# Kernel optimization log

Measured on AMD Instinct MI355X. Metric: run time of the kernel, lower is better.

## Reference

```python
import jax, jax.numpy as jnp
import numpy as np

LENGTHSCALES = np.array([0.1, 0.2, 0.5, 1.0, 2.0, 5.0, 10.0, 20.0], dtype=np.float32)
VALUE_DIM = 64
OUTPUT_DIM = 512
NUM_HEADS = len(LENGTHSCALES)


def setup_inputs() -> dict:
    key = jax.random.key(0)
    k1, k2, k3, k4, k5 = jax.random.split(key, 5)
    B, Lq, Lk, D = 4, 2048, 2048, 3
    query_positions = jax.random.normal(k1, (B, Lq, D), dtype=jnp.float32)
    key_positions = jax.random.normal(k2, (B, Lk, D), dtype=jnp.float32)
    values = jax.random.normal(k3, (B, Lk, NUM_HEADS, VALUE_DIM), dtype=jnp.float32)
    masked_elements = jax.random.randint(k4, (B, Lk), 0, 2) > 0
    # nn.Linear(value_dim*num_heads, output_dim, bias=False): weight [out, in]
    fan_in = VALUE_DIM * NUM_HEADS
    w_out = jax.random.uniform(k5, (OUTPUT_DIM, fan_in), dtype=jnp.float32,
                               minval=-1.0, maxval=1.0) / jnp.sqrt(fan_in)
    lengthscales = jnp.asarray(LENGTHSCALES)
    return {"query_positions": query_positions, "key_positions": key_positions,
            "values": values, "masked_elements": masked_elements,
            "lengthscales": lengthscales, "w_out": w_out}


def reference(query_positions, key_positions, values, masked_elements, lengthscales, w_out):
    # Euclidean distances via mm-trick (matches torch.cdist use_mm_for_euclid_dist)
    q2 = jnp.sum(query_positions ** 2, axis=-1)            # [B, Lq]
    k2 = jnp.sum(key_positions ** 2, axis=-1)              # [B, Lk]
    qk = jnp.einsum('bqd,bkd->bqk', query_positions, key_positions)
    d2 = jnp.maximum(q2[:, :, None] + k2[:, None, :] - 2.0 * qk, 0.0)
    distances = jnp.sqrt(d2)                               # [B, Lq, Lk]
    # per-head scaling + gaussian basis: exp(-(d/ls)^2)
    scaled = distances[:, None, :, :] / lengthscales[None, :, None, None]  # [B, H, Lq, Lk]
    scores = jnp.exp(-(scaled ** 2))
    scores = jnp.where(masked_elements[:, None, None, :], 0.0, scores)
    # masked sum-normalization
    scores = scores / (jnp.sum(jnp.abs(scores), axis=-1, keepdims=True) + 1e-5)
    # attend: values [B, Lk, H, V] -> [B, H, Lk, V]; then flatten heads -> [B, Lq, H*V]
    attended = jnp.einsum('bhqk,bkhv->bqhv', scores, values)
    B, Lq = attended.shape[0], attended.shape[1]
    flat = attended.reshape(B, Lq, -1)
    return flat @ w_out.T                                   # [B, Lq, output_dim]
```

## Files before the change

kernel.cpp:

```cpp
#include <hip/hip_runtime.h>
#include <math.h>

#define BB   4
#define LQ   2048
#define LK   2048
#define HD   8
#define VD   64
#define HV   512
#define OUTD 512
#define SP   72

typedef __attribute__((ext_vector_type(8))) short  bf16x8;
typedef __attribute__((ext_vector_type(4))) float  f32x4;

static __device__ __forceinline__ unsigned short f2bf(float f) {
    unsigned u = __builtin_bit_cast(unsigned, f);
    unsigned r = (u + 0x7fffu + ((u >> 16) & 1u)) >> 16;
    return (unsigned short)r;
}

__global__ __launch_bounds__(256) void cvt_vals(
    const float* __restrict__ vals, unsigned short* __restrict__ vals_t)
{
    __shared__ unsigned short st[64 * SP];
    const int tid = threadIdx.x;
    const int kt = blockIdx.x, h = blockIdx.y, b = blockIdx.z;

    const int k  = tid >> 2;
    const int vb = (tid & 3) * 16;
    const float* src = vals + (((size_t)(b * LK + kt * 64 + k) * HD + h)) * VD + vb;
    float4 f0 = *(const float4*)(src);
    float4 f1 = *(const float4*)(src + 4);
    float4 f2 = *(const float4*)(src + 8);
    float4 f3 = *(const float4*)(src + 12);
    const float fv[16] = {f0.x,f0.y,f0.z,f0.w, f1.x,f1.y,f1.z,f1.w,
                          f2.x,f2.y,f2.z,f2.w, f3.x,f3.y,f3.z,f3.w};
#pragma unroll
    for (int j = 0; j < 16; ++j) st[(vb + j) * SP + k] = f2bf(fv[j]);
    __syncthreads();

    const int v  = tid >> 2;
    const int kb = (tid & 3) * 16;
    uint4 o0 = *(const uint4*)&st[v * SP + kb];
    uint4 o1 = *(const uint4*)&st[v * SP + kb + 8];
    unsigned short* dst = vals_t + ((size_t)((b * HD + h) * VD + v)) * LK + kt * 64 + kb;
    *(uint4*)dst       = o0;
    *(uint4*)(dst + 8) = o1;
}

__global__ __launch_bounds__(256) void attend2(
    const float* __restrict__ qpos,
    const float* __restrict__ kpos,
    const unsigned short* __restrict__ vals_t,
    const int*   __restrict__ kmask,
    const float* __restrict__ ls,
    unsigned short* __restrict__ attended)
{
    __shared__ unsigned short sS[64 * SP];
    __shared__ unsigned short sV[64 * SP];
    __shared__ float s_kx[64], s_ky[64], s_kz[64];
    __shared__ float s_pd[256];
    __shared__ float s_inv[64];

    const int tid = threadIdx.x;
    const int qt = blockIdx.x, h = blockIdx.y, b = blockIdx.z;
    const int q0 = qt * 64;

    const float lsh  = ls[h];
    const float negc = -1.0f / (lsh * lsh);

    const int sq = tid >> 2;
    const int so = tid & 3;
    const float* qp = qpos + (size_t)(b * LQ + q0 + sq) * 3;
    const float qx = qp[0], qy = qp[1], qz = qp[2];

    const int vv = tid >> 3;
    const int vc = tid & 7;
    const unsigned short* vt_base = vals_t + (size_t)((b * HD + h) * VD) * LK;

    const int wave = tid >> 6;
    const int lane = tid & 63;
    const int ln = lane & 15, kq = lane >> 4;

    float pden = 0.f;
    f32x4 acc[4];
#pragma unroll
    for (int n = 0; n < 4; ++n) acc[n] = (f32x4){0.f, 0.f, 0.f, 0.f};

    for (int kt = 0; kt < LK; kt += 64) {
        __syncthreads();
        if (tid < 64) {
            const float* kp = kpos + (size_t)(b * LK + kt + tid) * 3;
            const int m = kmask[b * LK + kt + tid];
            float kx = kp[0];
            if (m) kx = 3.0e37f;
            s_kx[tid] = kx; s_ky[tid] = kp[1]; s_kz[tid] = kp[2];
        }
        {
            const unsigned short* src = vt_base + (size_t)vv * LK + kt + vc * 8;
            uint4 d0 = *(const uint4*)src;
            uint4 d1 = *(const uint4*)(src + (size_t)32 * LK);
            *(uint4*)&sV[vv * SP + vc * 8]        = d0;
            *(uint4*)&sV[(vv + 32) * SP + vc * 8] = d1;
        }
        __syncthreads();

#pragma unroll
        for (int p = 0; p < 2; ++p) {
            const int o = so + 4 * p;
            float kxa[8], kya[8], kza[8];
            *(float4*)&kxa[0] = *(const float4*)&s_kx[o * 8];
            *(float4*)&kxa[4] = *(const float4*)&s_kx[o * 8 + 4];
            *(float4*)&kya[0] = *(const float4*)&s_ky[o * 8];
            *(float4*)&kya[4] = *(const float4*)&s_ky[o * 8 + 4];
            *(float4*)&kza[0] = *(const float4*)&s_kz[o * 8];
            *(float4*)&kza[4] = *(const float4*)&s_kz[o * 8 + 4];
            unsigned pk[4];
            unsigned short us[8];
#pragma unroll
            for (int j = 0; j < 8; ++j) {
                const float dx = qx - kxa[j];
                const float dy = qy - kya[j];
                const float dz = qz - kza[j];
                const float d2 = fmaf(dx, dx, fmaf(dy, dy, dz * dz));
                const float sc = __expf(d2 * negc);
                pden += sc;
                us[j] = f2bf(sc);
            }
#pragma unroll
            for (int j = 0; j < 4; ++j)
                pk[j] = (unsigned)us[2 * j] | ((unsigned)us[2 * j + 1] << 16);
            *(uint4*)&sS[sq * SP + o * 8] = make_uint4(pk[0], pk[1], pk[2], pk[3]);
        }
        __syncthreads();

        {
            const unsigned short* ap = &sS[(wave * 16 + ln) * SP + kq * 8];
            const bf16x8 a0 = *(const bf16x8*)(ap);
            const bf16x8 a1 = *(const bf16x8*)(ap + 32);
#pragma unroll
            for (int n = 0; n < 4; ++n) {
                const unsigned short* bp = &sV[(n * 16 + ln) * SP + kq * 8];
                const bf16x8 b0 = *(const bf16x8*)(bp);
                const bf16x8 b1 = *(const bf16x8*)(bp + 32);
                acc[n] = __builtin_amdgcn_mfma_f32_16x16x32_bf16(a0, b0, acc[n], 0, 0, 0);
                acc[n] = __builtin_amdgcn_mfma_f32_16x16x32_bf16(a1, b1, acc[n], 0, 0, 0);
            }
        }
    }

    s_pd[tid] = pden;
    __syncthreads();
    if (tid < 64) {
        const float d = s_pd[tid * 4] + s_pd[tid * 4 + 1] +
                        s_pd[tid * 4 + 2] + s_pd[tid * 4 + 3];
        s_inv[tid] = 1.0f / (d + 1e-5f);
    }
    __syncthreads();

#pragma unroll
    for (int n = 0; n < 4; ++n) {
#pragma unroll
        for (int r = 0; r < 4; ++r) {
            const int q = wave * 16 + kq * 4 + r;
            const float val = acc[n][r] * s_inv[q];
            attended[(size_t)(b * LQ + q0 + q) * HV + h * VD + n * 16 + ln] = f2bf(val);
        }
    }
}

__global__ __launch_bounds__(256) void proj2(
    const unsigned short* __restrict__ A,
    const float* __restrict__ W,
    float* __restrict__ C)
{
    __shared__ unsigned short sA[64 * SP];
    __shared__ unsigned short sW[64 * SP];

    const int tid = threadIdx.x;
    const int n0 = blockIdx.x * 64, m0 = blockIdx.y * 64;
    const int wave = tid >> 6, lane = tid & 63;
    const int ln = lane & 15, kq = lane >> 4;

    const int am = tid >> 3, ac = tid & 7;
    const int wn = tid >> 2, wk = (tid & 3) * 16;

    f32x4 acc[4];
#pragma unroll
    for (int n = 0; n < 4; ++n) acc[n] = (f32x4){0.f, 0.f, 0.f, 0.f};

    for (int k0 = 0; k0 < 512; k0 += 64) {
        __syncthreads();
        {
            const unsigned short* asrc = A + (size_t)(m0 + am) * 512 + k0 + ac * 8;
            uint4 a0 = *(const uint4*)asrc;
            uint4 a1 = *(const uint4*)(asrc + (size_t)32 * 512);
            *(uint4*)&sA[am * SP + ac * 8]        = a0;
            *(uint4*)&sA[(am + 32) * SP + ac * 8] = a1;
        }
        {
            const float* wsrc = W + (size_t)(n0 + wn) * 512 + k0 + wk;
            float4 w0 = *(const float4*)(wsrc);
            float4 w1 = *(const float4*)(wsrc + 4);
            float4 w2 = *(const float4*)(wsrc + 8);
            float4 w3 = *(const float4*)(wsrc + 12);
            const float wf[16] = {w0.x,w0.y,w0.z,w0.w, w1.x,w1.y,w1.z,w1.w,
                                  w2.x,w2.y,w2.z,w2.w, w3.x,w3.y,w3.z,w3.w};
            unsigned pk[8];
#pragma unroll
            for (int j = 0; j < 8; ++j)
                pk[j] = (unsigned)f2bf(wf[2 * j]) | ((unsigned)f2bf(wf[2 * j + 1]) << 16);
            *(uint4*)&sW[wn * SP + wk]     = make_uint4(pk[0], pk[1], pk[2], pk[3]);
            *(uint4*)&sW[wn * SP + wk + 8] = make_uint4(pk[4], pk[5], pk[6], pk[7]);
        }
        __syncthreads();

        const unsigned short* ap = &sA[(wave * 16 + ln) * SP + kq * 8];
        const bf16x8 a0 = *(const bf16x8*)(ap);
        const bf16x8 a1 = *(const bf16x8*)(ap + 32);
#pragma unroll
        for (int n = 0; n < 4; ++n) {
            const unsigned short* bp = &sW[(n * 16 + ln) * SP + kq * 8];
            const bf16x8 b0 = *(const bf16x8*)(bp);
            const bf16x8 b1 = *(const bf16x8*)(bp + 32);
            acc[n] = __builtin_amdgcn_mfma_f32_16x16x32_bf16(a0, b0, acc[n], 0, 0, 0);
            acc[n] = __builtin_amdgcn_mfma_f32_16x16x32_bf16(a1, b1, acc[n], 0, 0, 0);
        }
    }

#pragma unroll
    for (int n = 0; n < 4; ++n) {
#pragma unroll
        for (int r = 0; r < 4; ++r) {
            C[(size_t)(m0 + wave * 16 + kq * 4 + r) * 512 + n0 + n * 16 + ln] = acc[n][r];
        }
    }
}

extern "C" void kernel_launch(void* const* d_in, const int* in_sizes, int n_in,
                              void* d_out, int out_size, void* d_ws, size_t ws_size,
                              hipStream_t stream) {
    const float* qpos  = (const float*)d_in[0];
    const float* kpos  = (const float*)d_in[1];
    const float* vals  = (const float*)d_in[2];
    const int*   kmask = (const int*)  d_in[3];
    const float* ls    = (const float*)d_in[4];
    const float* wout  = (const float*)d_in[5];
    float* out = (float*)d_out;

    unsigned short* vals_t   = (unsigned short*)d_ws;
    unsigned short* attended = vals_t + (size_t)4 * 1024 * 1024;

    cvt_vals<<<dim3(32, HD, BB), 256, 0, stream>>>(vals, vals_t);
    attend2 <<<dim3(32, HD, BB), 256, 0, stream>>>(qpos, kpos, vals_t, kmask, ls, attended);
    proj2   <<<dim3(OUTD / 64, (BB * LQ) / 64), 256, 0, stream>>>(attended, wout, out);
}
```

Measured before the change: 168.2 us.

## Restructure attention to four heads per block with register scores and pipelined loads

The attention kernel now gives each wave its own head and keeps the Gaussian scores in registers, feeding them straight into MFMA instead of staging them through shared memory. Value tiles and key positions are double-buffered with register prefetch, exp2 replaces exp, and bf16 packing truncates via a byte permute instead of rounding. The projection uses 128x128 tiles with a 4x4 MFMA tile per wave, and a separate pre-pass converts the weights to bf16. The aim is fewer barriers, less shared-memory traffic and less conversion ALU, at the cost of fewer blocks (256 for attention) and higher register pressure.

```diff
diff --git a/kernel.cpp b/kernel.cpp
--- a/kernel.cpp
+++ b/kernel.cpp
@@ -1,22 +1,34 @@
 #include <hip/hip_runtime.h>
 #include <math.h>
 
-#define BB   4
-#define LQ   2048
-#define LK   2048
-#define HD   8
-#define VD   64
-#define HV   512
-#define OUTD 512
-#define SP   72
-
-typedef __attribute__((ext_vector_type(8))) short  bf16x8;
-typedef __attribute__((ext_vector_type(4))) float  f32x4;
+#define BB 4
+#define LQ 2048
+#define LK 2048
+#define HD 8
+#define VD 64
+#define HV 512
+#define SP 72
+
+typedef __attribute__((ext_vector_type(8))) short bf16x8;
+typedef __attribute__((ext_vector_type(4))) float f32x4;
 
 static __device__ __forceinline__ unsigned short f2bf(float f) {
     unsigned u = __builtin_bit_cast(unsigned, f);
     unsigned r = (u + 0x7fffu + ((u >> 16) & 1u)) >> 16;
     return (unsigned short)r;
+}
+
+static __device__ __forceinline__ float fast_exp2(float x) {
+#if __has_builtin(__builtin_amdgcn_exp2f)
+    return __builtin_amdgcn_exp2f(x);
+#else
+    return __expf(x * 0.69314718f);
+#endif
+}
+
+static __device__ __forceinline__ unsigned pack_trunc(float even, float odd) {
+    return __builtin_amdgcn_perm(__builtin_bit_cast(unsigned, odd),
+                                 __builtin_bit_cast(unsigned, even), 0x07060302u);
 }
 
 __global__ __launch_bounds__(256) void cvt_vals(
@@ -48,7 +60,17 @@
     *(uint4*)(dst + 8) = o1;
 }
 
-__global__ __launch_bounds__(256) void attend2(
+__global__ __launch_bounds__(256) void cvt_w(
+    const float* __restrict__ w, unsigned short* __restrict__ wb)
+{
+    const int i = (blockIdx.x * 256 + threadIdx.x) * 4;
+    float4 f = *(const float4*)(w + i);
+    ushort4 o;
+    o.x = f2bf(f.x); o.y = f2bf(f.y); o.z = f2bf(f.z); o.w = f2bf(f.w);
+    *(ushort4*)(wb + i) = o;
+}
+
+__global__ __launch_bounds__(256, 1) void attend3(
     const float* __restrict__ qpos,
     const float* __restrict__ kpos,
     const unsigned short* __restrict__ vals_t,
@@ -56,185 +78,223 @@
     const float* __restrict__ ls,
     unsigned short* __restrict__ attended)
 {
-    __shared__ unsigned short sS[64 * SP];
-    __shared__ unsigned short sV[64 * SP];
-    __shared__ float s_kx[64], s_ky[64], s_kz[64];
-    __shared__ float s_pd[256];
-    __shared__ float s_inv[64];
-
-    const int tid = threadIdx.x;
-    const int qt = blockIdx.x, h = blockIdx.y, b = blockIdx.z;
+    __shared__ __align__(16) unsigned short sV[2][256 * SP];
+    __shared__ __align__(16) float skx[2][64], sky[2][64], skz[2][64];
+
+    const int tid  = threadIdx.x;
+    const int qt = blockIdx.x, hs = blockIdx.y, b = blockIdx.z;
     const int q0 = qt * 64;
-
-    const float lsh  = ls[h];
-    const float negc = -1.0f / (lsh * lsh);
-
-    const int sq = tid >> 2;
-    const int so = tid & 3;
-    const float* qp = qpos + (size_t)(b * LQ + q0 + sq) * 3;
-    const float qx = qp[0], qy = qp[1], qz = qp[2];
-
-    const int vv = tid >> 3;
-    const int vc = tid & 7;
-    const unsigned short* vt_base = vals_t + (size_t)((b * HD + h) * VD) * LK;
-
-    const int wave = tid >> 6;
-    const int lane = tid & 63;
+    const int wave = tid >> 6, lane = tid & 63;
     const int ln = lane & 15, kq = lane >> 4;
-
-    float pden = 0.f;
-    f32x4 acc[4];
-#pragma unroll
-    for (int n = 0; n < 4; ++n) acc[n] = (f32x4){0.f, 0.f, 0.f, 0.f};
-
-    for (int kt = 0; kt < LK; kt += 64) {
+    const int h = hs * 4 + wave;
+
+    const float lsh = ls[h];
+    const float ch  = -1.44269504f / (lsh * lsh);
+
+    float qx[4], qy[4], qz[4];
+#pragma unroll
+    for (int qs = 0; qs < 4; ++qs) {
+        const float* qp = qpos + (size_t)(b * LQ + q0 + qs * 16 + ln) * 3;
+        qx[qs] = qp[0]; qy[qs] = qp[1]; qz[qs] = qp[2];
+    }
+
+    const unsigned short* vsrc = vals_t + (size_t)((b * HD + h) * VD + lane) * LK;
+
+    uint4 vreg[8];
+    float kxr = 0.f, kyr = 0.f, kzr = 0.f;
+#pragma unroll
+    for (int j = 0; j < 8; ++j) vreg[j] = ((const uint4*)vsrc)[j];
+    if (tid < 64) {
+        const int idx = b * LK + tid;
+        kxr = kpos[(size_t)idx * 3];
+        kyr = kpos[(size_t)idx * 3 + 1];
+        kzr = kpos[(size_t)idx * 3 + 2];
+        if (kmask[idx]) kxr = 3.0e37f;
+    }
+    {
+        unsigned short* d = &sV[0][tid * SP];
+#pragma unroll
+        for (int j = 0; j < 8; ++j) *(uint4*)(d + j * 8) = vreg[j];
+        if (tid < 64) { skx[0][tid] = kxr; sky[0][tid] = kyr; skz[0][tid] = kzr; }
+    }
+    __syncthreads();
+
+    f32x4 acc[4][4];
+#pragma unroll
+    for (int i = 0; i < 4; ++i)
+#pragma unroll
+        for (int j = 0; j < 4; ++j) acc[i][j] = (f32x4){0.f, 0.f, 0.f, 0.f};
+    float pden[4] = {0.f, 0.f, 0.f, 0.f};
+
+    for (int t = 0; t < 32; ++t) {
+        const int cur = t & 1;
+        const int tn  = (t < 31) ? t + 1 : 0;
+
+        {
+            const unsigned short* s = vsrc + tn * 64;
+#pragma unroll
+            for (int j = 0; j < 8; ++j) vreg[j] = ((const uint4*)s)[j];
+        }
+        if (tid < 64) {
+            const int idx = b * LK + tn * 64 + tid;
+            kxr = kpos[(size_t)idx * 3];
+            kyr = kpos[(size_t)idx * 3 + 1];
+            kzr = kpos[(size_t)idx * 3 + 2];
+            if (kmask[idx]) kxr = 3.0e37f;
+        }
+
+        bf16x8 bfrag[4][2];
+#pragma unroll
+        for (int vt = 0; vt < 4; ++vt) {
+            const unsigned short* bp = &sV[cur][(wave * 64 + vt * 16 + ln) * SP + kq * 8];
+            bfrag[vt][0] = *(const bf16x8*)(bp);
+            bfrag[vt][1] = *(const bf16x8*)(bp + 32);
+        }
+
+        float kxa[16], kya[16], kza[16];
+        *(float4*)&kxa[0]  = *(const float4*)&skx[cur][kq * 8];
+        *(float4*)&kxa[4]  = *(const float4*)&skx[cur][kq * 8 + 4];
+        *(float4*)&kxa[8]  = *(const float4*)&skx[cur][kq * 8 + 32];
+        *(float4*)&kxa[12] = *(const float4*)&skx[cur][kq * 8 + 36];
+        *(float4*)&kya[0]  = *(const float4*)&sky[cur][kq * 8];
+        *(float4*)&kya[4]  = *(const float4*)&sky[cur][kq * 8 + 4];
+        *(float4*)&kya[8]  = *(const float4*)&sky[cur][kq * 8 + 32];
+        *(float4*)&kya[12] = *(const float4*)&sky[cur][kq * 8 + 36];
+        *(float4*)&kza[0]  = *(const float4*)&skz[cur][kq * 8];
+        *(float4*)&kza[4]  = *(const float4*)&skz[cur][kq * 8 + 4];
+        *(float4*)&kza[8]  = *(const float4*)&skz[cur][kq * 8 + 32];
+        *(float4*)&kza[12] = *(const float4*)&skz[cur][kq * 8 + 36];
+
+#pragma unroll
+        for (int qs = 0; qs < 4; ++qs) {
+            float s[16];
+#pragma unroll
+            for (int j = 0; j < 16; ++j) {
+                const float dx = qx[qs] - kxa[j];
+                const float dy = qy[qs] - kya[j];
+                const float dz = qz[qs] - kza[j];
+                const float d2 = fmaf(dx, dx, fmaf(dy, dy, dz * dz));
+                const float sc = fast_exp2(d2 * ch);
+                pden[qs] += sc;
+                s[j] = sc;
+            }
+            unsigned pk[8];
+#pragma unroll
+            for (int p = 0; p < 8; ++p) pk[p] = pack_trunc(s[2 * p], s[2 * p + 1]);
+            const bf16x8 a0 = __builtin_bit_cast(bf16x8, *(uint4*)&pk[0]);
+            const bf16x8 a1 = __builtin_bit_cast(bf16x8, *(uint4*)&pk[4]);
+#pragma unroll
+            for (int vt = 0; vt < 4; ++vt) {
+                acc[qs][vt] = __builtin_amdgcn_mfma_f32_16x16x32_bf16(a0, bfrag[vt][0], acc[qs][vt], 0, 0, 0);
+                acc[qs][vt] = __builtin_amdgcn_mfma_f32_16x16x32_bf16(a1, bfrag[vt][1], acc[qs][vt], 0, 0, 0);
+            }
+        }
+
+        {
+            const int nb = tn & 1;
+            unsigned short* d = &sV[nb][tid * SP];
+#pragma unroll
+            for (int j = 0; j < 8; ++j) *(uint4*)(d + j * 8) = vreg[j];
+            if (tid < 64) { skx[nb][tid] = kxr; sky[nb][tid] = kyr; skz[nb][tid] = kzr; }
+        }
         __syncthreads();
-        if (tid < 64) {
-            const float* kp = kpos + (size_t)(b * LK + kt + tid) * 3;
-            const int m = kmask[b * LK + kt + tid];
-            float kx = kp[0];
-            if (m) kx = 3.0e37f;
-            s_kx[tid] = kx; s_ky[tid] = kp[1]; s_kz[tid] = kp[2];
-        }
-        {
-            const unsigned short* src = vt_base + (size_t)vv * LK + kt + vc * 8;
-            uint4 d0 = *(const uint4*)src;
-            uint4 d1 = *(const uint4*)(src + (size_t)32 * LK);
-            *(uint4*)&sV[vv * SP + vc * 8]        = d0;
-            *(uint4*)&sV[(vv + 32) * SP + vc * 8] = d1;
-        }
-        __syncthreads();
-
-#pragma unroll
-        for (int p = 0; p < 2; ++p) {
-            const int o = so + 4 * p;
-            float kxa[8], kya[8], kza[8];
-            *(float4*)&kxa[0] = *(const float4*)&s_kx[o * 8];
-            *(float4*)&kxa[4] = *(const float4*)&s_kx[o * 8 + 4];
-            *(float4*)&kya[0] = *(const float4*)&s_ky[o * 8];
-            *(float4*)&kya[4] = *(const float4*)&s_ky[o * 8 + 4];
-            *(float4*)&kza[0] = *(const float4*)&s_kz[o * 8];
-            *(float4*)&kza[4] = *(const float4*)&s_kz[o * 8 + 4];
-            unsigned pk[4];
-            unsigned short us[8];
-#pragma unroll
-            for (int j = 0; j < 8; ++j) {
-                const float dx = qx - kxa[j];
-                const float dy = qy - kya[j];
-                const float dz = qz - kza[j];
-                const float d2 = fmaf(dx, dx, fmaf(dy, dy, dz * dz));
-                const float sc = __expf(d2 * negc);
-                pden += sc;
-                us[j] = f2bf(sc);
+    }
+
+    float inv[4];
+#pragma unroll
+    for (int qs = 0; qs < 4; ++qs) {
+        float v = pden[qs];
+        v += __shfl_xor(v, 16, 64);
+        v += __shfl_xor(v, 32, 64);
+        inv[qs] = 1.0f / (v + 1e-5f);
+    }
+    float ivq[4][4];
+#pragma unroll
+    for (int qs = 0; qs < 4; ++qs)
+#pragma unroll
+        for (int r = 0; r < 4; ++r) ivq[qs][r] = __shfl(inv[qs], kq * 4 + r, 64);
+
+#pragma unroll
+    for (int qs = 0; qs < 4; ++qs)
+#pragma unroll
+        for (int vt = 0; vt < 4; ++vt)
+#pragma unroll
+            for (int r = 0; r < 4; ++r) {
+                const int q = q0 + qs * 16 + kq * 4 + r;
+                attended[(size_t)(b * LQ + q) * HV + h * VD + vt * 16 + ln] =
+                    f2bf(acc[qs][vt][r] * ivq[qs][r]);
             }
-#pragma unroll
-            for (int j = 0; j < 4; ++j)
-                pk[j] = (unsigned)us[2 * j] | ((unsigned)us[2 * j + 1] << 16);
-            *(uint4*)&sS[sq * SP + o * 8] = make_uint4(pk[0], pk[1], pk[2], pk[3]);
-        }
-        __syncthreads();
-
-        {
-            const unsigned short* ap = &sS[(wave * 16 + ln) * SP + kq * 8];
-            const bf16x8 a0 = *(const bf16x8*)(ap);
-            const bf16x8 a1 = *(const bf16x8*)(ap + 32);
-#pragma unroll
-            for (int n = 0; n < 4; ++n) {
-                const unsigned short* bp = &sV[(n * 16 + ln) * SP + kq * 8];
-                const bf16x8 b0 = *(const bf16x8*)(bp);
-                const bf16x8 b1 = *(const bf16x8*)(bp + 32);
-                acc[n] = __builtin_amdgcn_mfma_f32_16x16x32_bf16(a0, b0, acc[n], 0, 0, 0);
-                acc[n] = __builtin_amdgcn_mfma_f32_16x16x32_bf16(a1, b1, acc[n], 0, 0, 0);
-            }
-        }
-    }
-
-    s_pd[tid] = pden;
-    __syncthreads();
-    if (tid < 64) {
-        const float d = s_pd[tid * 4] + s_pd[tid * 4 + 1] +
-                        s_pd[tid * 4 + 2] + s_pd[tid * 4 + 3];
-        s_inv[tid] = 1.0f / (d + 1e-5f);
-    }
-    __syncthreads();
-
-#pragma unroll
-    for (int n = 0; n < 4; ++n) {
-#pragma unroll
-        for (int r = 0; r < 4; ++r) {
-            const int q = wave * 16 + kq * 4 + r;
-            const float val = acc[n][r] * s_inv[q];
-            attended[(size_t)(b * LQ + q0 + q) * HV + h * VD + n * 16 + ln] = f2bf(val);
-        }
-    }
-}
-
-__global__ __launch_bounds__(256) void proj2(
+}
+
+__global__ __launch_bounds__(256, 1) void proj3(
     const unsigned short* __restrict__ A,
-    const float* __restrict__ W,
+    const unsigned short* __restrict__ Wb,
     float* __restrict__ C)
 {
-    __shared__ unsigned short sA[64 * SP];
-    __shared__ unsigned short sW[64 * SP];
+    __shared__ __align__(16) unsigned short sA[128 * SP];
+    __shared__ __align__(16) unsigned short sW[128 * SP];
 
     const int tid = threadIdx.x;
-    const int n0 = blockIdx.x * 64, m0 = blockIdx.y * 64;
+    const int n0 = blockIdx.x * 128, m0 = blockIdx.y * 128;
     const int wave = tid >> 6, lane = tid & 63;
     const int ln = lane & 15, kq = lane >> 4;
-
-    const int am = tid >> 3, ac = tid & 7;
-    const int wn = tid >> 2, wk = (tid & 3) * 16;
-
-    f32x4 acc[4];
-#pragma unroll
-    for (int n = 0; n < 4; ++n) acc[n] = (f32x4){0.f, 0.f, 0.f, 0.f};
+    const int mw = (wave >> 1) * 64, nw = (wave & 1) * 64;
+    const int sr = tid >> 1, sh = (tid & 1) * 32;
+
+    f32x4 acc[4][4];
+#pragma unroll
+    for (int i = 0; i < 4; ++i)
+#pragma unroll
+        for (int j = 0; j < 4; ++j) acc[i][j] = (f32x4){0.f, 0.f, 0.f, 0.f};
 
     for (int k0 = 0; k0 < 512; k0 += 64) {
         __syncthreads();
         {
-            const unsigned short* asrc = A + (size_t)(m0 + am) * 512 + k0 + ac * 8;
-            uint4 a0 = *(const uint4*)asrc;
-            uint4 a1 = *(const uint4*)(asrc + (size_t)32 * 512);
-            *(uint4*)&sA[am * SP + ac * 8]        = a0;
-            *(uint4*)&sA[(am + 32) * SP + ac * 8] = a1;
-        }
-        {
-            const float* wsrc = W + (size_t)(n0 + wn) * 512 + k0 + wk;
-            float4 w0 = *(const float4*)(wsrc);
-            float4 w1 = *(const float4*)(wsrc + 4);
-            float4 w2 = *(const float4*)(wsrc + 8);
-            float4 w3 = *(const float4*)(wsrc + 12);
-            const float wf[16] = {w0.x,w0.y,w0.z,w0.w, w1.x,w1.y,w1.z,w1.w,
-                                  w2.x,w2.y,w2.z,w2.w, w3.x,w3.y,w3.z,w3.w};
-            unsigned pk[8];
-#pragma unroll
-            for (int j = 0; j < 8; ++j)
-                pk[j] = (unsigned)f2bf(wf[2 * j]) | ((unsigned)f2bf(wf[2 * j + 1]) << 16);
-            *(uint4*)&sW[wn * SP + wk]     = make_uint4(pk[0], pk[1], pk[2], pk[3]);
-            *(uint4*)&sW[wn * SP + wk + 8] = make_uint4(pk[4], pk[5], pk[6], pk[7]);
+            const unsigned short* a = A  + (size_t)(m0 + sr) * 512 + k0 + sh;
+            const unsigned short* w = Wb + (size_t)(n0 + sr) * 512 + k0 + sh;
+            uint4 a0 = ((const uint4*)a)[0], a1 = ((const uint4*)a)[1],
+                  a2 = ((const uint4*)a)[2], a3 = ((const uint4*)a)[3];
+            uint4 w0 = ((const uint4*)w)[0], w1 = ((const uint4*)w)[1],
+                  w2 = ((const uint4*)w)[2], w3 = ((const uint4*)w)[3];
+            unsigned short* da = &sA[sr * SP + sh];
+            unsigned short* dw = &sW[sr * SP + sh];
+            ((uint4*)da)[0] = a0; ((uint4*)da)[1] = a1;
+            *(uint4*)(da + 16) = a2; *(uint4*)(da + 24) = a3;
+            ((uint4*)dw)[0] = w0; ((uint4*)dw)[1] = w1;
+            *(uint4*)(dw + 16) = w2; *(uint4*)(dw + 24) = w3;
         }
         __syncthreads();
 
-        const unsigned short* ap = &sA[(wave * 16 + ln) * SP + kq * 8];
-        const bf16x8 a0 = *(const bf16x8*)(ap);
-        const bf16x8 a1 = *(const bf16x8*)(ap + 32);
-#pragma unroll
-        for (int n = 0; n < 4; ++n) {
-            const unsigned short* bp = &sW[(n * 16 + ln) * SP + kq * 8];
-            const bf16x8 b0 = *(const bf16x8*)(bp);
-            const bf16x8 b1 = *(const bf16x8*)(bp + 32);
-            acc[n] = __builtin_amdgcn_mfma_f32_16x16x32_bf16(a0, b0, acc[n], 0, 0, 0);
-            acc[n] = __builtin_amdgcn_mfma_f32_16x16x32_bf16(a1, b1, acc[n], 0, 0, 0);
-        }
-    }
-
-#pragma unroll
-    for (int n = 0; n < 4; ++n) {
-#pragma unroll
-        for (int r = 0; r < 4; ++r) {
-            C[(size_t)(m0 + wave * 16 + kq * 4 + r) * 512 + n0 + n * 16 + ln] = acc[n][r];
-        }
-    }
+        bf16x8 af[4][2], bf[4][2];
+#pragma unroll
+        for (int mt = 0; mt < 4; ++mt) {
+            const unsigned short* ap = &sA[(mw + mt * 16 + ln) * SP + kq * 8];
+            af[mt][0] = *(const bf16x8*)(ap);
+            af[mt][1] = *(const bf16x8*)(ap + 32);
+        }
+#pragma unroll
+        for (int nt = 0; nt < 4; ++nt) {
+            const unsigned short* bp = &sW[(nw + nt * 16 + ln) * SP + kq * 8];
+            bf[nt][0] = *(const bf16x8*)(bp);
+            bf[nt][1] = *(const bf16x8*)(bp + 32);
+        }
+#pragma unroll
+        for (int mt = 0; mt < 4; ++mt)
+#pragma unroll
+            for (int nt = 0; nt < 4; ++nt) {
+                acc[mt][nt] = __builtin_amdgcn_mfma_f32_16x16x32_bf16(af[mt][0], bf[nt][0], acc[mt][nt], 0, 0, 0);
+                acc[mt][nt] = __builtin_amdgcn_mfma_f32_16x16x32_bf16(af[mt][1], bf[nt][1], acc[mt][nt], 0, 0, 0);
+            }
+    }
+
+#pragma unroll
+    for (int mt = 0; mt < 4; ++mt)
+#pragma unroll
+        for (int nt = 0; nt < 4; ++nt)
+#pragma unroll
+            for (int r = 0; r < 4; ++r)
+                C[(size_t)(m0 + mw + mt * 16 + kq * 4 + r) * 512 + n0 + nw + nt * 16 + ln] =
+                    acc[mt][nt][r];
 }
 
 extern "C" void kernel_launch(void* const* d_in, const int* in_sizes, int n_in,
@@ -250,8 +310,10 @@
 
     unsigned short* vals_t   = (unsigned short*)d_ws;
     unsigned short* attended = vals_t + (size_t)4 * 1024 * 1024;
+    unsigned short* w_bf     = vals_t + (size_t)8 * 1024 * 1024;
 
     cvt_vals<<<dim3(32, HD, BB), 256, 0, stream>>>(vals, vals_t);
-    attend2 <<<dim3(32, HD, BB), 256, 0, stream>>>(qpos, kpos, vals_t, kmask, ls, attended);
-    proj2   <<<dim3(OUTD / 64, (BB * LQ) / 64), 256, 0, stream>>>(attended, wout, out);
-}
+    cvt_w   <<<dim3(256), 256, 0, stream>>>(wout, w_bf);
+    attend3 <<<dim3(32, 2, BB), 256, 0, stream>>>(qpos, kpos, vals_t, kmask, ls, attended);
+    proj3   <<<dim3(4, 64), 256, 0, stream>>>(attended, w_bf, out);
+}
```

After: 189.5 us. 12.7% more time.
